# Kernel optimization log

Measured on AMD Instinct MI355X. Metric: run time of the kernel, lower is better.

## Reference

```python
import jax, jax.numpy as jnp
import numpy as np

EPS = 1e-7  # K.epsilon()
ROUTINGS = 3


def squash(v, axis=-1):
    s2 = jnp.sum(jnp.square(v), axis=axis, keepdims=True)
    scale = s2 / (1.0 + s2) / jnp.sqrt(s2 + EPS)
    return scale * v


def setup_inputs() -> dict:
    key = jax.random.key(0)
    k1, k2 = jax.random.split(key)
    B, I, D_IN = 64, 2048, 16
    J, D_OUT = 32, 32
    inputs = jax.random.normal(k1, (B, I, D_IN), dtype=jnp.float32)
    W = jax.random.normal(k2, (J, I, D_OUT, D_IN), dtype=jnp.float32) * 0.05
    return {"inputs": inputs, "W": W}


def reference(inputs, W):
    # u_hat[b,j,i,e] = sum_d inputs[b,i,d] * W[j,i,e,d]
    u_hat = jnp.einsum('bid,jied->bjie', inputs, W)  # [B, J, I, D_out]
    B, J, I, _ = u_hat.shape
    b = jnp.zeros((B, J, I), dtype=u_hat.dtype)
    outputs = None
    for r in range(ROUTINGS):
        c = jax.nn.softmax(b, axis=1)                 # softmax over output capsules J
        s = jnp.einsum('bji,bjie->bje', c, u_hat)     # weighted sum over input capsules
        outputs = squash(s)                           # [B, J, D_out]
        if r < ROUTINGS - 1:
            b = b + jnp.einsum('bje,bjie->bji', outputs, u_hat)
    return outputs
```

## Files before the change

kernel.cpp:

```cpp
#include <hip/hip_runtime.h>
#include <hip/hip_bf16.h>

#define NB 64
#define NI 2048
#define ND 16
#define NJ 32
#define NE 32
#define NIP (NI/2)
#define NKC 128
#define NSL NKC

typedef __attribute__((ext_vector_type(8))) short bfrag;
typedef __attribute__((ext_vector_type(4))) float f32x4;

__device__ inline unsigned pk2bf(float a, float b) {
    __hip_bfloat162 h = __float22bfloat162_rn(make_float2(a, b));
    return *reinterpret_cast<unsigned*>(&h);
}

template <int N>
__device__ inline float rot16_add(float v) {
    int r = __builtin_amdgcn_mov_dpp(__float_as_int(v), 0x120 + N, 0xf, 0xf, false);
    return v + __int_as_float(r);
}

__device__ inline unsigned scale_pair(unsigned u, float cc) {
    float f0 = __uint_as_float(u << 16);
    float f1 = __uint_as_float(u & 0xffff0000u);
    return pk2bf(f0 * cc, f1 * cc);
}

__global__ __launch_bounds__(256) void convxT_k(const float* __restrict__ x,
                                                short* __restrict__ xT)
{
    const int T = blockIdx.x * 256 + threadIdx.x;
    const int i = T >> 6, b = T & 63;
    const float4* src = reinterpret_cast<const float4*>(
        x + ((size_t)b * NI + i) * ND);
    float4 a0 = src[0], a1 = src[1], a2 = src[2], a3 = src[3];
    bfrag lo, hi;
    unsigned* lu = reinterpret_cast<unsigned*>(&lo);
    unsigned* hu = reinterpret_cast<unsigned*>(&hi);
    lu[0] = pk2bf(a0.x, a0.y); lu[1] = pk2bf(a0.z, a0.w);
    lu[2] = pk2bf(a1.x, a1.y); lu[3] = pk2bf(a1.z, a1.w);
    hu[0] = pk2bf(a2.x, a2.y); hu[1] = pk2bf(a2.z, a2.w);
    hu[2] = pk2bf(a3.x, a3.y); hu[3] = pk2bf(a3.z, a3.w);
    short* dst = xT + ((size_t)i * NB + b) * ND;
    *reinterpret_cast<bfrag*>(dst)     = lo;
    *reinterpret_cast<bfrag*>(dst + 8) = hi;
}

__global__ __launch_bounds__(512) void lgsm_k(
    const short* __restrict__ xT,
    const short* __restrict__ Wb,
    const float* __restrict__ Oacc,
    float* __restrict__ c)
{
    const int l    = blockIdx.x;
    const int grp  = l >> 5;
    const int bb   = (l >> 3) & 3;
    const int ic   = grp * 8 + (l & 7);
    const int b0   = bb * 16;
    const int i0   = ic * 16;
    const int t    = threadIdx.x;
    const int wv   = t >> 6;
    const int ln   = t & 63;
    const int m    = ln & 15;
    const int quad = ln >> 4;

    __shared__ float lp[NJ][16][16];

    float O0[4][4], O1[4][4];
#pragma unroll
    for (int jj = 0; jj < 4; ++jj) {
        const int j = wv * 4 + jj;
#pragma unroll
        for (int r = 0; r < 4; ++r) {
            const int b = b0 + quad * 4 + r;
            O0[jj][r] = Oacc[((size_t)b * NJ + j) * NE + m];
            O1[jj][r] = Oacc[((size_t)b * NJ + j) * NE + 16 + m];
        }
    }

    const int  bA  = b0 + m;
    const bool act = quad < 2;
    const int  d0  = quad * 8;

    for (int il = 0; il < 16; ++il) {
        const int i = i0 + il;
        const int ip = i >> 1, isel = i & 1;
        bfrag av = (bfrag)0;
        if (act) {
            av = *reinterpret_cast<const bfrag*>(
                xT + ((size_t)i * NB + bA) * ND + d0);
        }
#pragma unroll
        for (int jj = 0; jj < 4; ++jj) {
            const int j = wv * 4 + jj;
            bfrag bv0 = (bfrag)0, bv1 = (bfrag)0;
            if (act) {
                const short* wp = Wb + (((size_t)j * NIP + ip) * NE + m) * 32
                                     + isel * 16 + d0;
                bv0 = *reinterpret_cast<const bfrag*>(wp);
                bv1 = *reinterpret_cast<const bfrag*>(wp + 16 * 32);
            }
            f32x4 z = {0.f, 0.f, 0.f, 0.f};
            f32x4 U0 = __builtin_amdgcn_mfma_f32_16x16x32_bf16(av, bv0, z, 0, 0, 0);
            f32x4 U1 = __builtin_amdgcn_mfma_f32_16x16x32_bf16(av, bv1, z, 0, 0, 0);

            float v4[4];
#pragma unroll
            for (int r = 0; r < 4; ++r) {
                float v = fmaf(U0[r], O0[jj][r], U1[r] * O1[jj][r]);
                v = rot16_add<1>(v);
                v = rot16_add<2>(v);
                v = rot16_add<4>(v);
                v = rot16_add<8>(v);
                v4[r] = v;
            }
            if (m == 0) {
                *reinterpret_cast<float4*>(&lp[j][il][quad * 4]) =
                    make_float4(v4[0], v4[1], v4[2], v4[3]);
            }
        }
    }
    __syncthreads();

    if (t < 256) {
        const int i = t >> 4, b = t & 15;
        float v[NJ];
        float mx = -1e30f;
#pragma unroll
        for (int jx = 0; jx < NJ; ++jx) {
            v[jx] = lp[jx][i][b];
            mx = fmaxf(mx, v[jx]);
        }
        float sum = 0.f;
#pragma unroll
        for (int jx = 0; jx < NJ; ++jx) {
            v[jx] = __expf(v[jx] - mx);
            sum += v[jx];
        }
        const float inv = 1.0f / sum;
#pragma unroll
        for (int jx = 0; jx < NJ; ++jx)
            c[((size_t)jx * NI + i0 + i) * NB + b0 + b] = v[jx] * inv;
    }
}


#define WS_LOAD(P, itv)                                                        \
    {   const int ip_ = ip0 + (itv);                                           \
        const int ia_ = ip_ * 2 + isel;                                        \
        if constexpr (R0) {                                                    \
            const float* wp_ = Wsrc + (((size_t)j * NI + ia_) * NE + m) * ND + d0; \
            P##w0 = *reinterpret_cast<const float4*>(wp_);                     \
            P##w1 = *reinterpret_cast<const float4*>(wp_ + 4);                 \
            P##w2 = *reinterpret_cast<const float4*>(wp_ + 16 * ND);           \
            P##w3 = *reinterpret_cast<const float4*>(wp_ + 16 * ND + 4);       \
        } else {                                                               \
            const short* bp_ = Wb + (((size_t)j * NIP + ip_) * NE + m) * 32 + quad * 8; \
            P##bv0 = *reinterpret_cast<const bfrag*>(bp_);                     \
            P##bv1 = *reinterpret_cast<const bfrag*>(bp_ + 512);               \
            const float* cp_ = cbuf + ((size_t)j * NI + ia_) * NB + m;         \
            P##c0 = cp_[0];  P##c1 = cp_[16];                                  \
            P##c2 = cp_[32]; P##c3 = cp_[48];                                  \
        }                                                                      \
        const short* xp_ = xT + ((size_t)ia_ * NB + m) * ND + d0;              \
        P##x0 = *reinterpret_cast<const uint4*>(xp_);                          \
        P##x1 = *reinterpret_cast<const uint4*>(xp_ + 16 * ND);                \
        P##x2 = *reinterpret_cast<const uint4*>(xp_ + 32 * ND);                \
        P##x3 = *reinterpret_cast<const uint4*>(xp_ + 48 * ND);                \
    }

#define WS_MT(XV, CV, A0, A1)                                                  \
    {   const float cc_ = R0 ? (1.0f / NJ) : (CV);                             \
        bfrag av_;                                                             \
        unsigned* au_ = reinterpret_cast<unsigned*>(&av_);                     \
        au_[0] = scale_pair((XV).x, cc_); au_[1] = scale_pair((XV).y, cc_);    \
        au_[2] = scale_pair((XV).z, cc_); au_[3] = scale_pair((XV).w, cc_);    \
        A0 = __builtin_amdgcn_mfma_f32_16x16x32_bf16(av_, bv0_, A0, 0, 0, 0);  \
        A1 = __builtin_amdgcn_mfma_f32_16x16x32_bf16(av_, bv1_, A1, 0, 0, 0);  \
    }

#define WS_COMPUTE(P, itv)                                                     \
    {   bfrag bv0_, bv1_;                                                      \
        if constexpr (R0) {                                                    \
            unsigned* b0_ = reinterpret_cast<unsigned*>(&bv0_);                \
            unsigned* b1_ = reinterpret_cast<unsigned*>(&bv1_);                \
            b0_[0] = pk2bf(P##w0.x, P##w0.y); b0_[1] = pk2bf(P##w0.z, P##w0.w);\
            b0_[2] = pk2bf(P##w1.x, P##w1.y); b0_[3] = pk2bf(P##w1.z, P##w1.w);\
            b1_[0] = pk2bf(P##w2.x, P##w2.y); b1_[1] = pk2bf(P##w2.z, P##w2.w);\
            b1_[2] = pk2bf(P##w3.x, P##w3.y); b1_[3] = pk2bf(P##w3.z, P##w3.w);\
            short* wd_ = Wb + (((size_t)j * NIP + (ip0 + (itv))) * NE + m) * 32 + quad * 8; \
            *reinterpret_cast<bfrag*>(wd_)       = bv0_;                       \
            *reinterpret_cast<bfrag*>(wd_ + 512) = bv1_;                       \
        } else { bv0_ = P##bv0; bv1_ = P##bv1; }                               \
        WS_MT(P##x0, P##c0, a00, a01)                                          \
        WS_MT(P##x1, P##c1, a10, a11)                                          \
        WS_MT(P##x2, P##c2, a20, a21)                                          \
        WS_MT(P##x3, P##c3, a30, a31)                                          \
    }

template <bool R0>
__global__ __launch_bounds__(128) void wsum_k(
    const float* __restrict__ Wsrc,
    const short* __restrict__ xT,
    short* __restrict__ Wb,
    const float* __restrict__ cbuf,
    float* __restrict__ partial)
{
    const int l    = blockIdx.x;
    const int x    = l & 7;
    const int r    = l >> 3;
    const int j    = r & 31;
    const int kc   = x * 16 + (r >> 5);
    const int t    = threadIdx.x;
    const int wv   = t >> 6;
    const int ln   = t & 63;
    const int m    = ln & 15;
    const int quad = ln >> 4;
    const int isel = quad >> 1;
    const int d0   = (quad & 1) * 8;
    const int ip0  = kc * 8 + wv * 4;

    __shared__ float red[2048];

    f32x4 a00 = {0.f,0.f,0.f,0.f}, a01 = {0.f,0.f,0.f,0.f};
    f32x4 a10 = {0.f,0.f,0.f,0.f}, a11 = {0.f,0.f,0.f,0.f};
    f32x4 a20 = {0.f,0.f,0.f,0.f}, a21 = {0.f,0.f,0.f,0.f};
    f32x4 a30 = {0.f,0.f,0.f,0.f}, a31 = {0.f,0.f,0.f,0.f};

    bfrag  Abv0, Abv1, Bbv0, Bbv1;
    float4 Aw0, Aw1, Aw2, Aw3, Bw0, Bw1, Bw2, Bw3;
    uint4  Ax0, Ax1, Ax2, Ax3, Bx0, Bx1, Bx2, Bx3;
    float  Ac0, Ac1, Ac2, Ac3, Bc0, Bc1, Bc2, Bc3;

    WS_LOAD(A, 0)
    WS_LOAD(B, 1)
    WS_COMPUTE(A, 0)
    WS_LOAD(A, 2)
    WS_COMPUTE(B, 1)
    WS_LOAD(B, 3)
    WS_COMPUTE(A, 2)
    WS_COMPUTE(B, 3)

    if (wv == 1) {
        *reinterpret_cast<f32x4*>(red + 0 * 256 + ln * 4) = a00;
        *reinterpret_cast<f32x4*>(red + 1 * 256 + ln * 4) = a01;
        *reinterpret_cast<f32x4*>(red + 2 * 256 + ln * 4) = a10;
        *reinterpret_cast<f32x4*>(red + 3 * 256 + ln * 4) = a11;
        *reinterpret_cast<f32x4*>(red + 4 * 256 + ln * 4) = a20;
        *reinterpret_cast<f32x4*>(red + 5 * 256 + ln * 4) = a21;
        *reinterpret_cast<f32x4*>(red + 6 * 256 + ln * 4) = a30;
        *reinterpret_cast<f32x4*>(red + 7 * 256 + ln * 4) = a31;
    }
    __syncthreads();

    if (wv == 0) {
        float* pb = partial + ((size_t)kc * NJ + j) * 2048;
        a00 += *reinterpret_cast<const f32x4*>(red + 0 * 256 + ln * 4);
        a01 += *reinterpret_cast<const f32x4*>(red + 1 * 256 + ln * 4);
        a10 += *reinterpret_cast<const f32x4*>(red + 2 * 256 + ln * 4);
        a11 += *reinterpret_cast<const f32x4*>(red + 3 * 256 + ln * 4);
        a20 += *reinterpret_cast<const f32x4*>(red + 4 * 256 + ln * 4);
        a21 += *reinterpret_cast<const f32x4*>(red + 5 * 256 + ln * 4);
        a30 += *reinterpret_cast<const f32x4*>(red + 6 * 256 + ln * 4);
        a31 += *reinterpret_cast<const f32x4*>(red + 7 * 256 + ln * 4);
        *reinterpret_cast<f32x4*>(pb + 0 * 256 + ln * 4) = a00;
        *reinterpret_cast<f32x4*>(pb + 1 * 256 + ln * 4) = a01;
        *reinterpret_cast<f32x4*>(pb + 2 * 256 + ln * 4) = a10;
        *reinterpret_cast<f32x4*>(pb + 3 * 256 + ln * 4) = a11;
        *reinterpret_cast<f32x4*>(pb + 4 * 256 + ln * 4) = a20;
        *reinterpret_cast<f32x4*>(pb + 5 * 256 + ln * 4) = a21;
        *reinterpret_cast<f32x4*>(pb + 6 * 256 + ln * 4) = a30;
        *reinterpret_cast<f32x4*>(pb + 7 * 256 + ln * 4) = a31;
    }
}

__global__ __launch_bounds__(512) void rs_k(
    const float* __restrict__ partial,
    float* __restrict__ Oacc,
    float* __restrict__ out,
    int mode)
{
    const int G    = blockIdx.x * 512 + threadIdx.x;
    const int j    = G >> 11;
    const int g    = G & 2047;
    const int group = g >> 8;
    const int mt   = group >> 1;
    const int nt   = group & 1;
    const int lnn  = (g >> 2) & 63;
    const int m    = lnn & 15;
    const int quad = lnn >> 4;
    const int r    = g & 3;
    const int b    = mt * 16 + quad * 4 + r;
    const int e    = nt * 16 + m;

    float sum = 0.f;
#pragma unroll 8
    for (int sl = 0; sl < NSL; ++sl)
        sum += partial[((size_t)sl * NJ + j) * 2048 + g];

    __shared__ float lds[512];
    const int row = quad * 4 + r;
    lds[row * 32 + e] = sum;
    __syncthreads();
    const float* rp = &lds[row * 32];
    float p = 0.f;
#pragma unroll
    for (int ee = 0; ee < 32; ++ee) p = fmaf(rp[ee], rp[ee], p);

    const float scale = p / ((1.0f + p) * sqrtf(p + 1e-7f));
    const float o = scale * sum;
    const size_t off = ((size_t)b * NJ + j) * NE + e;
    if (mode == 2)      out[off]  = o;
    else if (mode == 1) Oacc[off] += o;
    else                Oacc[off] = o;
}

extern "C" void kernel_launch(void* const* d_in, const int* in_sizes, int n_in,
                              void* d_out, int out_size, void* d_ws, size_t ws_size,
                              hipStream_t stream)
{
    (void)in_sizes; (void)n_in; (void)out_size; (void)ws_size;
    const float* x = (const float*)d_in[0];
    const float* W = (const float*)d_in[1];
    float* out = (float*)d_out;

    float* Oacc = (float*)d_ws;
    float* c    = Oacc + NB * NJ * NE;
    float* part = c + (size_t)NJ * NI * NB;
    short* Wb   = (short*)(part + (size_t)NSL * NJ * 2048);
    short* xT   = Wb + (size_t)NJ * NIP * NE * 32;

    convxT_k<<<(NI * NB) / 256, 256, 0, stream>>>(x, xT);

    wsum_k<true><<<NJ * NKC, 128, 0, stream>>>(W, xT, Wb, c, part);
    rs_k<<<65536 / 512, 512, 0, stream>>>(part, Oacc, out, 0);

    lgsm_k<<<512, 512, 0, stream>>>(xT, Wb, Oacc, c);
    wsum_k<false><<<NJ * NKC, 128, 0, stream>>>(W, xT, Wb, c, part);
    rs_k<<<65536 / 512, 512, 0, stream>>>(part, Oacc, out, 1);

    lgsm_k<<<512, 512, 0, stream>>>(xT, Wb, Oacc, c);
    wsum_k<false><<<NJ * NKC, 128, 0, stream>>>(W, xT, Wb, c, part);
    rs_k<<<65536 / 512, 512, 0, stream>>>(part, Oacc, out, 2);
}
```

Measured before the change: 356.0 us.

## Fuse logit, softmax and weighted sum into one routing kernel

```diff
diff --git a/kernel.cpp b/kernel.cpp
--- a/kernel.cpp
+++ b/kernel.cpp
@@ -50,11 +50,11 @@
     *reinterpret_cast<bfrag*>(dst + 8) = hi;
 }
 
-__global__ __launch_bounds__(512) void lgsm_k(
+__global__ __launch_bounds__(512) void fwd_k(
     const short* __restrict__ xT,
     const short* __restrict__ Wb,
     const float* __restrict__ Oacc,
-    float* __restrict__ c)
+    float* __restrict__ part)
 {
     const int l    = blockIdx.x;
     const int grp  = l >> 5;
@@ -68,7 +68,7 @@
     const int m    = ln & 15;
     const int quad = ln >> 4;
 
-    __shared__ float lp[NJ][16][16];
+    __shared__ float lsm[2][NJ][16];
 
     float O0[4][4], O1[4][4];
 #pragma unroll
@@ -86,7 +86,14 @@
     const bool act = quad < 2;
     const int  d0  = quad * 8;
 
+    float s0[4][4], s1[4][4];
+#pragma unroll
+    for (int jj = 0; jj < 4; ++jj)
+#pragma unroll
+        for (int r = 0; r < 4; ++r) { s0[jj][r] = 0.f; s1[jj][r] = 0.f; }
+
     for (int il = 0; il < 16; ++il) {
+        const int buf = il & 1;
         const int i = i0 + il;
         const int ip = i >> 1, isel = i & 1;
         bfrag av = (bfrag)0;
@@ -94,6 +101,7 @@
             av = *reinterpret_cast<const bfrag*>(
                 xT + ((size_t)i * NB + bA) * ND + d0);
         }
+
 #pragma unroll
         for (int jj = 0; jj < 4; ++jj) {
             const int j = wv * 4 + jj;
@@ -119,52 +127,106 @@
                 v4[r] = v;
             }
             if (m == 0) {
-                *reinterpret_cast<float4*>(&lp[j][il][quad * 4]) =
+                *reinterpret_cast<float4*>(&lsm[buf][j][quad * 4]) =
                     make_float4(v4[0], v4[1], v4[2], v4[3]);
             }
         }
-    }
-    __syncthreads();
-
-    if (t < 256) {
-        const int i = t >> 4, b = t & 15;
-        float v[NJ];
-        float mx = -1e30f;
-#pragma unroll
-        for (int jx = 0; jx < NJ; ++jx) {
-            v[jx] = lp[jx][i][b];
-            mx = fmaxf(mx, v[jx]);
-        }
-        float sum = 0.f;
-#pragma unroll
-        for (int jx = 0; jx < NJ; ++jx) {
-            v[jx] = __expf(v[jx] - mx);
-            sum += v[jx];
-        }
-        const float inv = 1.0f / sum;
-#pragma unroll
-        for (int jx = 0; jx < NJ; ++jx)
-            c[((size_t)jx * NI + i0 + i) * NB + b0 + b] = v[jx] * inv;
-    }
+        __syncthreads();
+
+        if (t < 16) {
+            float mx = -1e30f;
+#pragma unroll
+            for (int jx = 0; jx < NJ; ++jx) mx = fmaxf(mx, lsm[buf][jx][t]);
+            float sum = 0.f;
+#pragma unroll
+            for (int jx = 0; jx < NJ; ++jx) {
+                const float e = __expf(lsm[buf][jx][t] - mx);
+                lsm[buf][jx][t] = e;
+                sum += e;
+            }
+            const float inv = 1.0f / sum;
+#pragma unroll
+            for (int jx = 0; jx < NJ; ++jx) lsm[buf][jx][t] *= inv;
+        }
+        __syncthreads();
+
+#pragma unroll
+        for (int jj = 0; jj < 4; ++jj) {
+            const int j = wv * 4 + jj;
+            bfrag bv0 = (bfrag)0, bv1 = (bfrag)0;
+            if (act) {
+                const short* wp = Wb + (((size_t)j * NIP + ip) * NE + m) * 32
+                                     + isel * 16 + d0;
+                bv0 = *reinterpret_cast<const bfrag*>(wp);
+                bv1 = *reinterpret_cast<const bfrag*>(wp + 16 * 32);
+            }
+            f32x4 z = {0.f, 0.f, 0.f, 0.f};
+            f32x4 U0 = __builtin_amdgcn_mfma_f32_16x16x32_bf16(av, bv0, z, 0, 0, 0);
+            f32x4 U1 = __builtin_amdgcn_mfma_f32_16x16x32_bf16(av, bv1, z, 0, 0, 0);
+#pragma unroll
+            for (int r = 0; r < 4; ++r) {
+                const float cv = lsm[buf][j][quad * 4 + r];
+                s0[jj][r] = fmaf(cv, U0[r], s0[jj][r]);
+                s1[jj][r] = fmaf(cv, U1[r], s1[jj][r]);
+            }
+        }
+    }
+
+    float* base = part + ((size_t)(bb * 128 + ic) * NJ) * 512;
+#pragma unroll
+    for (int jj = 0; jj < 4; ++jj) {
+        const int j = wv * 4 + jj;
+#pragma unroll
+        for (int r = 0; r < 4; ++r) {
+            float* p = base + (size_t)j * 512 + (quad * 4 + r) * 32 + m;
+            p[0]  = s0[jj][r];
+            p[16] = s1[jj][r];
+        }
+    }
+}
+
+__global__ __launch_bounds__(512) void rs2_k(
+    const float* __restrict__ part,
+    float* __restrict__ Oacc,
+    float* __restrict__ out,
+    int mode)
+{
+    const int G = blockIdx.x * 512 + threadIdx.x;
+    const int e = G & 31;
+    const int j = (G >> 5) & 31;
+    const int b = G >> 10;
+    const int bb = b >> 4, bl = b & 15;
+
+    const float* p = part + ((size_t)(bb * 128) * NJ + j) * 512 + bl * 32 + e;
+    float sum = 0.f;
+#pragma unroll 8
+    for (int icx = 0; icx < 128; ++icx)
+        sum += p[(size_t)icx * NJ * 512];
+
+    float q = sum * sum;
+    q = rot16_add<1>(q);
+    q = rot16_add<2>(q);
+    q = rot16_add<4>(q);
+    q = rot16_add<8>(q);
+    q += __shfl_xor(q, 16);
+
+    const float scale = q / ((1.0f + q) * sqrtf(q + 1e-7f));
+    const float o = scale * sum;
+    const size_t off = ((size_t)b * NJ + j) * NE + e;
+    if (mode == 2) out[off] = o;
+    else           Oacc[off] += o;
 }
 
 
 #define WS_LOAD(P, itv)                                                        \
     {   const int ip_ = ip0 + (itv);                                           \
         const int ia_ = ip_ * 2 + isel;                                        \
-        if constexpr (R0) {                                                    \
+        {                                                                      \
             const float* wp_ = Wsrc + (((size_t)j * NI + ia_) * NE + m) * ND + d0; \
             P##w0 = *reinterpret_cast<const float4*>(wp_);                     \
             P##w1 = *reinterpret_cast<const float4*>(wp_ + 4);                 \
             P##w2 = *reinterpret_cast<const float4*>(wp_ + 16 * ND);           \
             P##w3 = *reinterpret_cast<const float4*>(wp_ + 16 * ND + 4);       \
-        } else {                                                               \
-            const short* bp_ = Wb + (((size_t)j * NIP + ip_) * NE + m) * 32 + quad * 8; \
-            P##bv0 = *reinterpret_cast<const bfrag*>(bp_);                     \
-            P##bv1 = *reinterpret_cast<const bfrag*>(bp_ + 512);               \
-            const float* cp_ = cbuf + ((size_t)j * NI + ia_) * NB + m;         \
-            P##c0 = cp_[0];  P##c1 = cp_[16];                                  \
-            P##c2 = cp_[32]; P##c3 = cp_[48];                                  \
         }                                                                      \
         const short* xp_ = xT + ((size_t)ia_ * NB + m) * ND + d0;              \
         P##x0 = *reinterpret_cast<const uint4*>(xp_);                          \
@@ -173,8 +235,8 @@
         P##x3 = *reinterpret_cast<const uint4*>(xp_ + 48 * ND);                \
     }
 
-#define WS_MT(XV, CV, A0, A1)                                                  \
-    {   const float cc_ = R0 ? (1.0f / NJ) : (CV);                             \
+#define WS_MT(XV, A0, A1)                                                      \
+    {   const float cc_ = 1.0f / NJ;                                           \
         bfrag av_;                                                             \
         unsigned* au_ = reinterpret_cast<unsigned*>(&av_);                     \
         au_[0] = scale_pair((XV).x, cc_); au_[1] = scale_pair((XV).y, cc_);    \
@@ -185,7 +247,7 @@
 
 #define WS_COMPUTE(P, itv)                                                     \
     {   bfrag bv0_, bv1_;                                                      \
-        if constexpr (R0) {                                                    \
+        {                                                                      \
             unsigned* b0_ = reinterpret_cast<unsigned*>(&bv0_);                \
             unsigned* b1_ = reinterpret_cast<unsigned*>(&bv1_);                \
             b0_[0] = pk2bf(P##w0.x, P##w0.y); b0_[1] = pk2bf(P##w0.z, P##w0.w);\
@@ -195,19 +257,17 @@
             short* wd_ = Wb + (((size_t)j * NIP + (ip0 + (itv))) * NE + m) * 32 + quad * 8; \
             *reinterpret_cast<bfrag*>(wd_)       = bv0_;                       \
             *reinterpret_cast<bfrag*>(wd_ + 512) = bv1_;                       \
-        } else { bv0_ = P##bv0; bv1_ = P##bv1; }                               \
-        WS_MT(P##x0, P##c0, a00, a01)                                          \
-        WS_MT(P##x1, P##c1, a10, a11)                                          \
-        WS_MT(P##x2, P##c2, a20, a21)                                          \
-        WS_MT(P##x3, P##c3, a30, a31)                                          \
-    }
-
-template <bool R0>
+        }                                                                      \
+        WS_MT(P##x0, a00, a01)                                                 \
+        WS_MT(P##x1, a10, a11)                                                 \
+        WS_MT(P##x2, a20, a21)                                                 \
+        WS_MT(P##x3, a30, a31)                                                 \
+    }
+
 __global__ __launch_bounds__(128) void wsum_k(
     const float* __restrict__ Wsrc,
     const short* __restrict__ xT,
     short* __restrict__ Wb,
-    const float* __restrict__ cbuf,
     float* __restrict__ partial)
 {
     const int l    = blockIdx.x;
@@ -231,10 +291,8 @@
     f32x4 a20 = {0.f,0.f,0.f,0.f}, a21 = {0.f,0.f,0.f,0.f};
     f32x4 a30 = {0.f,0.f,0.f,0.f}, a31 = {0.f,0.f,0.f,0.f};
 
-    bfrag  Abv0, Abv1, Bbv0, Bbv1;
     float4 Aw0, Aw1, Aw2, Aw3, Bw0, Bw1, Bw2, Bw3;
     uint4  Ax0, Ax1, Ax2, Ax3, Bx0, Bx1, Bx2, Bx3;
-    float  Ac0, Ac1, Ac2, Ac3, Bc0, Bc1, Bc2, Bc3;
 
     WS_LOAD(A, 0)
     WS_LOAD(B, 1)
@@ -329,21 +387,18 @@
     float* out = (float*)d_out;
 
     float* Oacc = (float*)d_ws;
-    float* c    = Oacc + NB * NJ * NE;
-    float* part = c + (size_t)NJ * NI * NB;
+    float* part = Oacc + NB * NJ * NE;
     short* Wb   = (short*)(part + (size_t)NSL * NJ * 2048);
     short* xT   = Wb + (size_t)NJ * NIP * NE * 32;
 
     convxT_k<<<(NI * NB) / 256, 256, 0, stream>>>(x, xT);
 
-    wsum_k<true><<<NJ * NKC, 128, 0, stream>>>(W, xT, Wb, c, part);
+    wsum_k<<<NJ * NKC, 128, 0, stream>>>(W, xT, Wb, part);
     rs_k<<<65536 / 512, 512, 0, stream>>>(part, Oacc, out, 0);
 
-    lgsm_k<<<512, 512, 0, stream>>>(xT, Wb, Oacc, c);
-    wsum_k<false><<<NJ * NKC, 128, 0, stream>>>(W, xT, Wb, c, part);
-    rs_k<<<65536 / 512, 512, 0, stream>>>(part, Oacc, out, 1);
-
-    lgsm_k<<<512, 512, 0, stream>>>(xT, Wb, Oacc, c);
-    wsum_k<false><<<NJ * NKC, 128, 0, stream>>>(W, xT, Wb, c, part);
-    rs_k<<<65536 / 512, 512, 0, stream>>>(part, Oacc, out, 2);
-}
+    fwd_k<<<512, 512, 0, stream>>>(xT, Wb, Oacc, part);
+    rs2_k<<<65536 / 512, 512, 0, stream>>>(part, Oacc, out, 1);
+
+    fwd_k<<<512, 512, 0, stream>>>(xT, Wb, Oacc, part);
+    rs2_k<<<65536 / 512, 512, 0, stream>>>(part, Oacc, out, 2);
+}
```

Result: slower. 494.9 us (+39.0%).
